# Kernel tuning notes

Measured on AMD Instinct MI355X. Metric: run time of the kernel, lower is better.

The kernel has to match this reference:

```python
import jax, jax.numpy as jnp
import numpy as np

B, S, D = 2, 2048, 2048
NH, NKV, HD = 16, 4, 128
EPS = 1e-6


def rmsnorm(x, w, eps=EPS):
    # torch.nn.RMSNorm: x * rsqrt(mean(x^2) + eps) * weight
    ms = jnp.mean(jnp.square(x), axis=-1, keepdims=True)
    return x * jax.lax.rsqrt(ms + eps) * w


def apply_rotary_emb(x, freqs_cis):
    # x: (B, S, H, HD); freqs_cis: (S, HD//2, 2) -> pairwise complex rotation (gpt-fast style)
    xs = x.reshape(*x.shape[:-1], -1, 2)          # (B,S,H,HD//2,2)
    fc = freqs_cis[None, :, None, :, :]           # (1,S,1,HD//2,2)
    xr, xi = xs[..., 0], xs[..., 1]
    fr, fi = fc[..., 0], fc[..., 1]
    out = jnp.stack([xr * fr - xi * fi, xi * fr + xr * fi], axis=-1)
    return out.reshape(x.shape)


def setup_inputs() -> dict:
    key = jax.random.key(0)
    ks = jax.random.split(key, 4)
    x = jax.random.normal(ks[0], (B, S, D), dtype=jnp.float32)
    freqs_cis = jax.random.normal(ks[1], (S, HD // 2, 2), dtype=jnp.float32)
    wqkv = jax.random.normal(ks[2], ((NH + 2 * NKV) * HD, D), dtype=jnp.float32) * (D ** -0.5)
    wo = jax.random.normal(ks[3], (NH * HD, D), dtype=jnp.float32).T * ((NH * HD) ** -0.5)
    wo = jnp.asarray(wo)  # (D, NH*HD) torch layout (out,in)
    q_norm_w = jnp.ones((HD,), dtype=jnp.float32)
    k_norm_w = jnp.ones((HD,), dtype=jnp.float32)
    return {"x": x, "freqs_cis": freqs_cis, "wqkv": wqkv, "wo": wo,
            "q_norm_w": q_norm_w, "k_norm_w": k_norm_w}


def reference(x, freqs_cis, wqkv, wo, q_norm_w, k_norm_w):
    b, s, _ = x.shape
    q_size, kv_size = NH * HD, NKV * HD
    qkv = jnp.einsum('bsd,ed->bse', x, wqkv)  # fused QKV projection
    q, k, v = jnp.split(qkv, [q_size, q_size + kv_size], axis=-1)
    q = q.reshape(b, s, NH, HD)
    k = k.reshape(b, s, NKV, HD)
    v = v.reshape(b, s, NKV, HD)
    q = rmsnorm(q, q_norm_w)
    k = rmsnorm(k, k_norm_w)
    q = apply_rotary_emb(q, freqs_cis)
    k = apply_rotary_emb(k, freqs_cis)
    # GQA: repeat_interleave KV heads to NH
    rep = NH // NKV
    k = jnp.repeat(k, rep, axis=2)  # (b,s,NH,HD)
    v = jnp.repeat(v, rep, axis=2)
    scale = 1.0 / np.sqrt(HD)
    scores = jnp.einsum('bqhd,bkhd->bhqk', q, k) * scale
    causal = jnp.tril(jnp.ones((s, s), dtype=bool))
    scores = jnp.where(causal[None, None], scores, -jnp.inf)
    attn = jax.nn.softmax(scores, axis=-1)
    y = jnp.einsum('bhqk,bkhd->bqhd', attn, v)
    y = y.reshape(b, s, q_size)
    return jnp.einsum('bse,de->bsd', y, wo)
```

## Files before the change

kernel.cpp:

```cpp
#include <hip/hip_runtime.h>
#include <math.h>

constexpr int B_ = 2, S_ = 2048, D_ = 2048, NH_ = 16, NKV_ = 4, HD_ = 128;
constexpr int EQKV_ = (NH_ + 2 * NKV_) * HD_;
constexpr int M_ = B_ * S_;
constexpr float EPS_ = 1e-6f;
constexpr float QSCALE_ = 0.08838834764831845f;

typedef __attribute__((ext_vector_type(8))) short bf16x8;
typedef __attribute__((ext_vector_type(4))) float f32x4;
typedef __attribute__((address_space(1))) unsigned int gu32;
typedef __attribute__((address_space(3))) unsigned int lu32;

__device__ inline ushort f2bf(float f) {
    unsigned u = __float_as_uint(f);
    return (ushort)((u + 0x7FFF + ((u >> 16) & 1)) >> 16);
}

__global__ __launch_bounds__(256) void pack_bf16(
    const float* __restrict__ in, ushort* __restrict__ out, int n4)
{
    int i = blockIdx.x * 256 + threadIdx.x;
    if (i >= n4) return;
    float4 f = ((const float4*)in)[i];
    ushort4 u;
    u.x = f2bf(f.x); u.y = f2bf(f.y); u.z = f2bf(f.z); u.w = f2bf(f.w);
    ((ushort4*)out)[i] = u;
}

__global__ __launch_bounds__(256) void gemm_nt_bf16(
    const ushort* __restrict__ A, const ushort* __restrict__ W,
    float* __restrict__ C, int M, int N, int K)
{
    __shared__ ushort As[128 * 32];
    __shared__ ushort Bs[128 * 32];
    const int t = threadIdx.x;
    const int wave = t >> 6, lane = t & 63;
    const int m0 = blockIdx.y * 128, n0 = blockIdx.x * 128;
    const int wm = (wave >> 1) * 64, wn = (wave & 1) * 64;
    const int lrow = lane & 15, lquad = lane >> 4;

    f32x4 acc[4][4];
#pragma unroll
    for (int i = 0; i < 4; ++i)
#pragma unroll
        for (int j = 0; j < 4; ++j) acc[i][j] = (f32x4){0.f, 0.f, 0.f, 0.f};

    for (int k0 = 0; k0 < K; k0 += 32) {
        __syncthreads();
#pragma unroll
        for (int i = 0; i < 2; ++i) {
            int chunk = t + 256 * i;
            int row = chunk >> 2, seg = chunk & 3;
            int ubase = (wave * 64 + 256 * i) * 8;
            __builtin_amdgcn_global_load_lds(
                (const gu32*)(A + (size_t)(m0 + row) * K + k0 + seg * 8),
                (lu32*)(As + ubase), 16, 0, 0);
            __builtin_amdgcn_global_load_lds(
                (const gu32*)(W + (size_t)(n0 + row) * K + k0 + seg * 8),
                (lu32*)(Bs + ubase), 16, 0, 0);
        }
        __syncthreads();

        bf16x8 af[4], bf[4];
#pragma unroll
        for (int i = 0; i < 4; ++i) {
            af[i] = *(const bf16x8*)(As + (wm + i * 16 + lrow) * 32 + lquad * 8);
            bf[i] = *(const bf16x8*)(Bs + (wn + i * 16 + lrow) * 32 + lquad * 8);
        }
#pragma unroll
        for (int i = 0; i < 4; ++i)
#pragma unroll
            for (int j = 0; j < 4; ++j)
                acc[i][j] = __builtin_amdgcn_mfma_f32_16x16x32_bf16(
                    af[i], bf[j], acc[i][j], 0, 0, 0);
    }
#pragma unroll
    for (int i = 0; i < 4; ++i)
#pragma unroll
        for (int j = 0; j < 4; ++j) {
            float* cp = C + (size_t)(m0 + wm + i * 16 + lquad * 4) * N
                          + n0 + wn + j * 16 + lrow;
#pragma unroll
            for (int r = 0; r < 4; ++r) cp[(size_t)r * N] = acc[i][j][r];
        }
}

__global__ __launch_bounds__(256) void gemm_qkv_fused(
    const ushort* __restrict__ A,
    const ushort* __restrict__ W,
    const float* __restrict__ freqs,
    const float* __restrict__ qw, const float* __restrict__ kw,
    ushort* __restrict__ qo, ushort* __restrict__ ko, ushort* __restrict__ vo,
    int K)
{
    __shared__ __align__(16) ushort smem[128 * 136];
    __shared__ float rsbuf[256];
    ushort* As = smem;
    ushort* Bs = smem + 4096;
    ushort* Lt = smem;

    const int t = threadIdx.x;
    const int wave = t >> 6, lane = t & 63;
    const int m0 = blockIdx.y * 128, n0 = blockIdx.x * 128;
    const int wm = (wave >> 1) * 64, wn = (wave & 1) * 64;
    const int half = wave & 1;
    const int lrow = lane & 15, lquad = lane >> 4;
    const int head = n0 >> 7;
    const int b = m0 >> 11, s0 = m0 & (S_ - 1);

    f32x4 acc[4][4];
#pragma unroll
    for (int i = 0; i < 4; ++i)
#pragma unroll
        for (int j = 0; j < 4; ++j) acc[i][j] = (f32x4){0.f, 0.f, 0.f, 0.f};

    for (int k0 = 0; k0 < K; k0 += 32) {
        __syncthreads();
#pragma unroll
        for (int i = 0; i < 2; ++i) {
            int chunk = t + 256 * i;
            int row = chunk >> 2, seg = chunk & 3;
            int ubase = (wave * 64 + 256 * i) * 8;
            __builtin_amdgcn_global_load_lds(
                (const gu32*)(A + (size_t)(m0 + row) * K + k0 + seg * 8),
                (lu32*)(As + ubase), 16, 0, 0);
            __builtin_amdgcn_global_load_lds(
                (const gu32*)(W + (size_t)(n0 + row) * K + k0 + seg * 8),
                (lu32*)(Bs + ubase), 16, 0, 0);
        }
        __syncthreads();

        bf16x8 af[4], bf[4];
#pragma unroll
        for (int i = 0; i < 4; ++i) {
            af[i] = *(const bf16x8*)(As + (wm + i * 16 + lrow) * 32 + lquad * 8);
            bf[i] = *(const bf16x8*)(Bs + (wn + i * 16 + lrow) * 32 + lquad * 8);
        }
#pragma unroll
        for (int i = 0; i < 4; ++i)
#pragma unroll
            for (int j = 0; j < 4; ++j)
                acc[i][j] = __builtin_amdgcn_mfma_f32_16x16x32_bf16(
                    af[i], bf[j], acc[i][j], 0, 0, 0);
    }
    __syncthreads();

    float part[4][4];
    if (head < NH_ + NKV_) {
#pragma unroll
        for (int i = 0; i < 4; ++i)
#pragma unroll
            for (int r = 0; r < 4; ++r) {
                float p = acc[i][0][r] * acc[i][0][r]
                        + acc[i][1][r] * acc[i][1][r]
                        + acc[i][2][r] * acc[i][2][r]
                        + acc[i][3][r] * acc[i][3][r];
#pragma unroll
                for (int off = 1; off < 16; off <<= 1) p += __shfl_xor(p, off);
                part[i][r] = p;
                if (lrow == 0)
                    rsbuf[half * 128 + wm + i * 16 + lquad * 4 + r] = p;
            }
    }
    __syncthreads();

    if (head < NH_ + NKV_) {
        const float* nw = (head < NH_) ? qw : kw;
        float wv[4];
#pragma unroll
        for (int j = 0; j < 4; ++j) wv[j] = nw[wn + j * 16 + lrow];
#pragma unroll
        for (int i = 0; i < 4; ++i)
#pragma unroll
            for (int r = 0; r < 4; ++r) {
                const int rowid = wm + i * 16 + lquad * 4 + r;
                const int s = s0 + rowid;
                const float total = part[i][r] + rsbuf[(half ^ 1) * 128 + rowid];
                const float rs = rsqrtf(total * (1.0f / HD_) + EPS_);
#pragma unroll
                for (int j = 0; j < 4; ++j) {
                    const int d = wn + j * 16 + lrow;
                    const float xn = acc[i][j][r] * rs * wv[j];
                    const float other = __shfl_xor(xn, 1);
                    const float fr = freqs[s * HD_ + (d & ~1)];
                    const float fi = freqs[s * HD_ + (d & ~1) + 1];
                    float out = (d & 1) ? fmaf(xn, fr, other * fi)
                                        : fmaf(xn, fr, -other * fi);
                    if (head < NH_) out *= QSCALE_;
                    Lt[rowid * 136 + d] = f2bf(out);
                }
            }
    } else {
#pragma unroll
        for (int i = 0; i < 4; ++i)
#pragma unroll
            for (int j = 0; j < 4; ++j)
#pragma unroll
                for (int r = 0; r < 4; ++r)
                    Lt[(wn + j * 16 + lrow) * 136 + wm + i * 16 + lquad * 4 + r]
                        = f2bf(acc[i][j][r]);
    }
    __syncthreads();

    const int g = t >> 4, lx16 = t & 15;
    if (head < NH_) {
        ushort* dst0 = qo + ((size_t)(b * NH_ + head) * S_ + s0) * HD_;
#pragma unroll
        for (int it = 0; it < 8; ++it) {
            const int rowid = it * 16 + g;
            uint4 v = *(const uint4*)(Lt + rowid * 136 + lx16 * 8);
            *(uint4*)(dst0 + (size_t)rowid * HD_ + lx16 * 8) = v;
        }
    } else if (head < NH_ + NKV_) {
        const int kh = head - NH_;
        ushort* dst0 = ko + ((size_t)(b * NKV_ + kh) * S_ + s0) * HD_;
#pragma unroll
        for (int it = 0; it < 8; ++it) {
            const int rowid = it * 16 + g;
            uint4 v = *(const uint4*)(Lt + rowid * 136 + lx16 * 8);
            *(uint4*)(dst0 + (size_t)rowid * HD_ + lx16 * 8) = v;
        }
    } else {
        const int vh = head - (NH_ + NKV_);
        ushort* dst0 = vo + ((size_t)(b * NKV_ + vh) * HD_) * S_ + s0;
#pragma unroll
        for (int it = 0; it < 8; ++it) {
            const int rowid = it * 16 + g;
            uint4 v = *(const uint4*)(Lt + rowid * 136 + lx16 * 8);
            *(uint4*)(dst0 + (size_t)rowid * S_ + lx16 * 8) = v;
        }
    }
}

__global__ __launch_bounds__(512, 4) void flash_attn_mfma(
    const ushort* __restrict__ Q,
    const ushort* __restrict__ K,
    const ushort* __restrict__ V,
    ushort* __restrict__ Y,
    float* __restrict__ OP,
    float* __restrict__ ML)
{
    __shared__ __align__(16) ushort Ks[4 * 64 * 32];
    __shared__ __align__(16) ushort Vs[2 * 128 * 32];
    __shared__ __align__(16) ushort Ps[8 * 16 * 72];

    const int t = threadIdx.x, w = t >> 6, lane = t & 63;
    const int lx = lane & 15, quad = lane >> 4;
    const int h = blockIdx.y, b = blockIdx.z;

    const int gx = blockIdx.x;
    int qb, halfsel, tk0, tk1;
    bool split;
    if (gx < 22) {
        split = true;
        qb = 15 - (gx >> 1);
        halfsel = gx & 1;
        const int h0 = qb + 1;
        tk0 = halfsel ? h0 : 0;
        tk1 = halfsel ? 2 * qb + 2 : h0;
    } else {
        split = false;
        qb = 26 - gx;
        halfsel = 0;
        tk0 = 0;
        tk1 = 2 * qb + 2;
    }
    const int q0 = qb * 128;
    const int kvh = h >> 2;

    const int srow8 = lane >> 3, sseg8 = lane & 7;
    const int fsw = (srow8 >> 1) & 3;
    const int slotw = ((sseg8 & 3) ^ fsw) * 8;
    const int krow = w * 8 + srow8;
    const int d0 = w * 8 + srow8;
    ushort* kdst = Ks + (sseg8 >> 2) * 2048 + krow * 32 + slotw;
    ushort* vdst = Vs + (sseg8 >> 2) * 4096 + d0 * 32 + slotw;
    const ushort* ksrc = K + ((size_t)(b * NKV_ + kvh) * S_ + krow) * HD_
                           + sseg8 * 8;
    const ushort* vsrc = V + ((size_t)(b * NKV_ + kvh) * HD_ + d0) * S_
                           + sseg8 * 8;
    const int rslot = (quad ^ ((lx >> 1) & 3)) * 8;

    const ushort* qb_ = Q + ((size_t)(b * NH_ + h) * S_ + q0) * HD_;
    bf16x8 aq[4];
#pragma unroll
    for (int ks = 0; ks < 4; ++ks)
        aq[ks] = *(const bf16x8*)(qb_ + (size_t)(w * 16 + lx) * HD_ + ks * 32 + quad * 8);

    f32x4 o[8];
#pragma unroll
    for (int j = 0; j < 8; ++j) o[j] = (f32x4){0.f, 0.f, 0.f, 0.f};
    float mrow[4] = {-INFINITY, -INFINITY, -INFINITY, -INFINITY};
    float lp[4] = {0.f, 0.f, 0.f, 0.f};

    uint4 kr0, kr1, vr0, vr1;
    {
        const size_t kf = (size_t)tk0 * 64;
        kr0 = *(const uint4*)(ksrc + kf * HD_);
        kr1 = *(const uint4*)(ksrc + kf * HD_ + 64);
        vr0 = *(const uint4*)(vsrc + kf);
        vr1 = *(const uint4*)(vsrc + (size_t)64 * S_ + kf);
    }

    for (int tk = tk0; tk < tk1; ++tk) {
        const int k0 = tk * 64;
        asm volatile("s_barrier" ::: "memory");
        *(uint4*)(kdst +    0) = kr0;
        *(uint4*)(kdst + 4096) = kr1;
        *(uint4*)(vdst +    0) = vr0;
        *(uint4*)(vdst + 2048) = vr1;
        asm volatile("s_waitcnt lgkmcnt(0)" ::: "memory");
        asm volatile("s_barrier" ::: "memory");

        if (tk + 1 < tk1) {
            const size_t kf = (size_t)(k0 + 64);
            kr0 = *(const uint4*)(ksrc + kf * HD_);
            kr1 = *(const uint4*)(ksrc + kf * HD_ + 64);
            vr0 = *(const uint4*)(vsrc + kf);
            vr1 = *(const uint4*)(vsrc + (size_t)64 * S_ + kf);
        }

        f32x4 s[4];
#pragma unroll
        for (int j = 0; j < 4; ++j) s[j] = (f32x4){0.f, 0.f, 0.f, 0.f};
        __builtin_amdgcn_s_setprio(1);
#pragma unroll
        for (int ks = 0; ks < 4; ++ks) {
#pragma unroll
            for (int j = 0; j < 4; ++j) {
                bf16x8 bk = *(const bf16x8*)(Ks + ks * 2048 + (j * 16 + lx) * 32 + rslot);
                s[j] = __builtin_amdgcn_mfma_f32_16x16x32_bf16(aq[ks], bk, s[j], 0, 0, 0);
            }
        }
        __builtin_amdgcn_s_setprio(0);

        const int qrow_base = q0 + w * 16 + quad * 4;
        if (k0 + 63 > q0 + w * 16) {
#pragma unroll
            for (int reg = 0; reg < 4; ++reg) {
                const int qrow = qrow_base + reg;
#pragma unroll
                for (int j = 0; j < 4; ++j)
                    if (k0 + lx + 16 * j > qrow) s[j][reg] = -INFINITY;
            }
        }

        float rmx[4];
        bool need = false;
#pragma unroll
        for (int reg = 0; reg < 4; ++reg) {
            rmx[reg] = fmaxf(fmaxf(s[0][reg], s[1][reg]),
                             fmaxf(s[2][reg], s[3][reg]));
            need |= (rmx[reg] > mrow[reg] + 8.0f);
        }
        if (__any(need)) {
#pragma unroll
            for (int reg = 0; reg < 4; ++reg) {
                float rm = rmx[reg];
#pragma unroll
                for (int off = 1; off < 16; off <<= 1)
                    rm = fmaxf(rm, __shfl_xor(rm, off));
                const float mn = fmaxf(mrow[reg], rm);
                const float alpha = __expf(mrow[reg] - mn);
                mrow[reg] = mn;
                lp[reg] *= alpha;
#pragma unroll
                for (int j = 0; j < 8; ++j) o[j][reg] *= alpha;
            }
        }
#pragma unroll
        for (int reg = 0; reg < 4; ++reg) {
#pragma unroll
            for (int j = 0; j < 4; ++j) {
                const float p = __expf(s[j][reg] - mrow[reg]);
                lp[reg] += p;
                Ps[w * 1152 + (quad * 4 + reg) * 72 + lx + 16 * j] = f2bf(p);
            }
        }

        bf16x8 ap[2];
#pragma unroll
        for (int ks2 = 0; ks2 < 2; ++ks2)
            ap[ks2] = *(const bf16x8*)(Ps + w * 1152 + lx * 72 + ks2 * 32 + quad * 8);
        __builtin_amdgcn_s_setprio(1);
#pragma unroll
        for (int jd = 0; jd < 8; ++jd) {
#pragma unroll
            for (int ks2 = 0; ks2 < 2; ++ks2) {
                bf16x8 bv = *(const bf16x8*)(Vs + ks2 * 4096 + (jd * 16 + lx) * 32 + rslot);
                o[jd] = __builtin_amdgcn_mfma_f32_16x16x32_bf16(ap[ks2], bv, o[jd], 0, 0, 0);
            }
        }
        __builtin_amdgcn_s_setprio(0);
    }

#pragma unroll
    for (int reg = 0; reg < 4; ++reg) {
        float l = lp[reg];
#pragma unroll
        for (int off = 1; off < 16; off <<= 1) l += __shfl_xor(l, off);
        lp[reg] = l;
    }
    if (!split) {
#pragma unroll
        for (int reg = 0; reg < 4; ++reg) {
            const float inv = 1.0f / lp[reg];
            const size_t yb = (size_t)(b * S_ + q0 + w * 16 + quad * 4 + reg) * (NH_ * HD_)
                            + h * HD_ + lx;
#pragma unroll
            for (int jd = 0; jd < 8; ++jd)
                Y[yb + jd * 16] = f2bf(o[jd][reg] * inv);
        }
    } else {
        const int sp = ((b * NH_ + h) * 11 + (qb - 5)) * 2 + halfsel;
        float* mlb = ML + (size_t)sp * 256;
#pragma unroll
        for (int reg = 0; reg < 4; ++reg) {
            const int row = w * 16 + quad * 4 + reg;
            if (lx == 0) {
                mlb[row] = mrow[reg];
                mlb[128 + row] = lp[reg];
            }
            float* ob = OP + ((size_t)sp * 128 + row) * 128 + lx;
#pragma unroll
            for (int jd = 0; jd < 8; ++jd)
                ob[jd * 16] = o[jd][reg];
        }
    }
}

__global__ __launch_bounds__(256) void attn_combine(
    const float* __restrict__ OP, const float* __restrict__ ML,
    ushort* __restrict__ Y)
{
    const int gx = blockIdx.x, h = blockIdx.y, b = blockIdx.z;
    const int qb = 5 + gx;
    const int q0 = qb * 128;
    const int sp0 = ((b * NH_ + h) * 11 + gx) * 2;
    const float* ml0 = ML + (size_t)sp0 * 256;
    const float* ml1 = ML + (size_t)(sp0 + 1) * 256;
    const float* o0 = OP + (size_t)sp0 * 128 * 128;
    const float* o1 = OP + (size_t)(sp0 + 1) * 128 * 128;
    const int d = threadIdx.x & 127, rg = threadIdx.x >> 7;
#pragma unroll
    for (int r = rg; r < 128; r += 2) {
        const float m0 = ml0[r], l0 = ml0[128 + r];
        const float m1 = ml1[r], l1 = ml1[128 + r];
        const float m = fmaxf(m0, m1);
        const float w0 = __expf(m0 - m), w1 = __expf(m1 - m);
        const float inv = 1.0f / (l0 * w0 + l1 * w1);
        const float v = (o0[r * 128 + d] * w0 + o1[r * 128 + d] * w1) * inv;
        Y[((size_t)(b * S_ + q0 + r)) * (NH_ * HD_) + h * HD_ + d] = f2bf(v);
    }
}

extern "C" void kernel_launch(void* const* d_in, const int* in_sizes, int n_in,
                              void* d_out, int out_size, void* d_ws, size_t ws_size,
                              hipStream_t stream)
{
    const float* x     = (const float*)d_in[0];
    const float* freqs = (const float*)d_in[1];
    const float* wqkv  = (const float*)d_in[2];
    const float* wo    = (const float*)d_in[3];
    const float* qw    = (const float*)d_in[4];
    const float* kw    = (const float*)d_in[5];
    float* out = (float*)d_out;

    char* ws = (char*)d_ws;
    ushort* qbf    = (ushort*)(ws + 0);
    ushort* kbf    = (ushort*)(ws + 16777216);
    ushort* vtb    = (ushort*)(ws + 20971520);
    ushort* ybf    = (ushort*)(ws + 25165824);
    ushort* wobf   = (ushort*)(ws + 41943040);
    ushort* wqkvbf = (ushort*)(ws + 50331648);
    ushort* xbf    = (ushort*)(ws + 83886080);
    float*  OP     = (float*)(ws + 50331648);
    float*  ML     = (float*)(ws + 96468992);

    pack_bf16<<<(M_ * D_ / 4 + 255) / 256, 256, 0, stream>>>(x, xbf, M_ * D_ / 4);
    pack_bf16<<<(EQKV_ * D_ / 4 + 255) / 256, 256, 0, stream>>>(wqkv, wqkvbf,
                                                                EQKV_ * D_ / 4);
    gemm_qkv_fused<<<dim3(EQKV_ / 128, M_ / 128), 256, 0, stream>>>(
        xbf, wqkvbf, freqs, qw, kw, qbf, kbf, vtb, D_);
    pack_bf16<<<(D_ * NH_ * HD_ / 4 + 255) / 256, 256, 0, stream>>>(
        wo, wobf, D_ * NH_ * HD_ / 4);
    flash_attn_mfma<<<dim3(27, NH_, B_), 512, 0, stream>>>(qbf, kbf, vtb, ybf,
                                                           OP, ML);
    attn_combine<<<dim3(11, NH_, B_), 256, 0, stream>>>(OP, ML, ybf);
    gemm_nt_bf16<<<dim3(D_ / 128, M_ / 128), 256, 0, stream>>>(
        ybf, wobf, out, M_, D_, NH_ * HD_);
}
```

Measured before the change: 353.8 us.

## Double-buffer LDS tiles in QKV and output GEMMs to overlap loads with MFMA

Both GEMM kernels now use two LDS stages. Each loop iteration issues the global-to-LDS load of the next K-slice before running the MFMAs on the current slice, and uses a single waitcnt plus barrier per stage instead of two syncthreads. Load addresses are also precomputed outside the loop. This doubles the LDS used for the tiles, which may lower occupancy, in exchange for hiding global load latency behind compute.

```diff
diff --git a/kernel.cpp b/kernel.cpp
--- a/kernel.cpp
+++ b/kernel.cpp
@@ -28,53 +28,74 @@
     ((ushort4*)out)[i] = u;
 }
 
+#define GSTAGE(k0s, ASP, BSP) do {                                            \
+    __builtin_amdgcn_global_load_lds((const gu32*)(Aa0 + (k0s)),              \
+                                     (lu32*)((ASP) + ub0), 16, 0, 0);         \
+    __builtin_amdgcn_global_load_lds((const gu32*)(Aa1 + (k0s)),              \
+                                     (lu32*)((ASP) + ub1), 16, 0, 0);         \
+    __builtin_amdgcn_global_load_lds((const gu32*)(Wa0 + (k0s)),              \
+                                     (lu32*)((BSP) + ub0), 16, 0, 0);         \
+    __builtin_amdgcn_global_load_lds((const gu32*)(Wa1 + (k0s)),              \
+                                     (lu32*)((BSP) + ub1), 16, 0, 0);         \
+} while (0)
+
+#define GCOMPUTE(ASP, BSP) do {                                               \
+    bf16x8 af[4], bfr[4];                                                     \
+    _Pragma("unroll")                                                         \
+    for (int i_ = 0; i_ < 4; ++i_) {                                          \
+        af[i_]  = *(const bf16x8*)((ASP) + (wm + i_ * 16 + lrow) * 32 + lquad * 8); \
+        bfr[i_] = *(const bf16x8*)((BSP) + (wn + i_ * 16 + lrow) * 32 + lquad * 8); \
+    }                                                                         \
+    _Pragma("unroll")                                                         \
+    for (int i_ = 0; i_ < 4; ++i_)                                            \
+        _Pragma("unroll")                                                     \
+        for (int j_ = 0; j_ < 4; ++j_)                                        \
+            acc[i_][j_] = __builtin_amdgcn_mfma_f32_16x16x32_bf16(            \
+                af[i_], bfr[j_], acc[i_][j_], 0, 0, 0);                       \
+} while (0)
+
+#define GBAR() do {                                                           \
+    asm volatile("s_waitcnt vmcnt(0)" ::: "memory");                          \
+    __builtin_amdgcn_s_barrier();                                             \
+} while (0)
+
 __global__ __launch_bounds__(256) void gemm_nt_bf16(
     const ushort* __restrict__ A, const ushort* __restrict__ W,
     float* __restrict__ C, int M, int N, int K)
 {
-    __shared__ ushort As[128 * 32];
-    __shared__ ushort Bs[128 * 32];
+    __shared__ __align__(16) ushort As[2 * 4096];
+    __shared__ __align__(16) ushort Bs[2 * 4096];
     const int t = threadIdx.x;
     const int wave = t >> 6, lane = t & 63;
     const int m0 = blockIdx.y * 128, n0 = blockIdx.x * 128;
     const int wm = (wave >> 1) * 64, wn = (wave & 1) * 64;
     const int lrow = lane & 15, lquad = lane >> 4;
 
+    const ushort* Aa0 = A + (size_t)(m0 + (t >> 2)) * K + (t & 3) * 8;
+    const ushort* Aa1 = Aa0 + (size_t)64 * K;
+    const ushort* Wa0 = W + (size_t)(n0 + (t >> 2)) * K + (t & 3) * 8;
+    const ushort* Wa1 = Wa0 + (size_t)64 * K;
+    const int ub0 = wave * 512, ub1 = wave * 512 + 2048;
+    ushort* As0 = As;      ushort* As1 = As + 4096;
+    ushort* Bs0 = Bs;      ushort* Bs1 = Bs + 4096;
+
     f32x4 acc[4][4];
 #pragma unroll
     for (int i = 0; i < 4; ++i)
 #pragma unroll
         for (int j = 0; j < 4; ++j) acc[i][j] = (f32x4){0.f, 0.f, 0.f, 0.f};
 
-    for (int k0 = 0; k0 < K; k0 += 32) {
-        __syncthreads();
-#pragma unroll
-        for (int i = 0; i < 2; ++i) {
-            int chunk = t + 256 * i;
-            int row = chunk >> 2, seg = chunk & 3;
-            int ubase = (wave * 64 + 256 * i) * 8;
-            __builtin_amdgcn_global_load_lds(
-                (const gu32*)(A + (size_t)(m0 + row) * K + k0 + seg * 8),
-                (lu32*)(As + ubase), 16, 0, 0);
-            __builtin_amdgcn_global_load_lds(
-                (const gu32*)(W + (size_t)(n0 + row) * K + k0 + seg * 8),
-                (lu32*)(Bs + ubase), 16, 0, 0);
-        }
-        __syncthreads();
-
-        bf16x8 af[4], bf[4];
-#pragma unroll
-        for (int i = 0; i < 4; ++i) {
-            af[i] = *(const bf16x8*)(As + (wm + i * 16 + lrow) * 32 + lquad * 8);
-            bf[i] = *(const bf16x8*)(Bs + (wn + i * 16 + lrow) * 32 + lquad * 8);
-        }
-#pragma unroll
-        for (int i = 0; i < 4; ++i)
-#pragma unroll
-            for (int j = 0; j < 4; ++j)
-                acc[i][j] = __builtin_amdgcn_mfma_f32_16x16x32_bf16(
-                    af[i], bf[j], acc[i][j], 0, 0, 0);
-    }
+    GSTAGE(0, As0, Bs0);
+    GBAR();
+    for (int k0 = 0; k0 < K; k0 += 64) {
+        GSTAGE(k0 + 32, As1, Bs1);
+        GCOMPUTE(As0, Bs0);
+        GBAR();
+        if (k0 + 64 < K) GSTAGE(k0 + 64, As0, Bs0);
+        GCOMPUTE(As1, Bs1);
+        GBAR();
+    }
+
 #pragma unroll
     for (int i = 0; i < 4; ++i)
 #pragma unroll
@@ -94,10 +115,12 @@
     ushort* __restrict__ qo, ushort* __restrict__ ko, ushort* __restrict__ vo,
     int K)
 {
-    __shared__ __align__(16) ushort smem[128 * 136];
+    __shared__ __align__(16) ushort smem[17408];
     __shared__ float rsbuf[256];
-    ushort* As = smem;
-    ushort* Bs = smem + 4096;
+    ushort* As0 = smem;
+    ushort* As1 = smem + 4096;
+    ushort* Bs0 = smem + 8192;
+    ushort* Bs1 = smem + 12288;
     ushort* Lt = smem;
 
     const int t = threadIdx.x;
@@ -109,40 +132,27 @@
     const int head = n0 >> 7;
     const int b = m0 >> 11, s0 = m0 & (S_ - 1);
 
+    const ushort* Aa0 = A + (size_t)(m0 + (t >> 2)) * K + (t & 3) * 8;
+    const ushort* Aa1 = Aa0 + (size_t)64 * K;
+    const ushort* Wa0 = W + (size_t)(n0 + (t >> 2)) * K + (t & 3) * 8;
+    const ushort* Wa1 = Wa0 + (size_t)64 * K;
+    const int ub0 = wave * 512, ub1 = wave * 512 + 2048;
+
     f32x4 acc[4][4];
 #pragma unroll
     for (int i = 0; i < 4; ++i)
 #pragma unroll
         for (int j = 0; j < 4; ++j) acc[i][j] = (f32x4){0.f, 0.f, 0.f, 0.f};
 
-    for (int k0 = 0; k0 < K; k0 += 32) {
-        __syncthreads();
-#pragma unroll
-        for (int i = 0; i < 2; ++i) {
-            int chunk = t + 256 * i;
-            int row = chunk >> 2, seg = chunk & 3;
-            int ubase = (wave * 64 + 256 * i) * 8;
-            __builtin_amdgcn_global_load_lds(
-                (const gu32*)(A + (size_t)(m0 + row) * K + k0 + seg * 8),
-                (lu32*)(As + ubase), 16, 0, 0);
-            __builtin_amdgcn_global_load_lds(
-                (const gu32*)(W + (size_t)(n0 + row) * K + k0 + seg * 8),
-                (lu32*)(Bs + ubase), 16, 0, 0);
-        }
-        __syncthreads();
-
-        bf16x8 af[4], bf[4];
-#pragma unroll
-        for (int i = 0; i < 4; ++i) {
-            af[i] = *(const bf16x8*)(As + (wm + i * 16 + lrow) * 32 + lquad * 8);
-            bf[i] = *(const bf16x8*)(Bs + (wn + i * 16 + lrow) * 32 + lquad * 8);
-        }
-#pragma unroll
-        for (int i = 0; i < 4; ++i)
-#pragma unroll
-            for (int j = 0; j < 4; ++j)
-                acc[i][j] = __builtin_amdgcn_mfma_f32_16x16x32_bf16(
-                    af[i], bf[j], acc[i][j], 0, 0, 0);
+    GSTAGE(0, As0, Bs0);
+    GBAR();
+    for (int k0 = 0; k0 < K; k0 += 64) {
+        GSTAGE(k0 + 32, As1, Bs1);
+        GCOMPUTE(As0, Bs0);
+        GBAR();
+        if (k0 + 64 < K) GSTAGE(k0 + 64, As0, Bs0);
+        GCOMPUTE(As1, Bs1);
+        GBAR();
     }
     __syncthreads();
 
```

Result: slower. 375.0 us (+6.0%).
